# Kernel tuning notes

Hardware: AMD Instinct MI355X
Metric: run time of the kernel (lower is better)

## Reference

```python
import jax, jax.numpy as jnp
import numpy as np

B, L, IN, HID, D3 = 32, 8192, 512, 512, 128

def setup_inputs() -> dict:
    key = jax.random.key(0)
    ks = jax.random.split(key, 7)
    s_in = 1.0 / np.sqrt(IN)
    s_h = 1.0 / np.sqrt(HID)
    return {
        'inputs': jax.random.normal(ks[0], (B, IN), jnp.float32),
        'context': jax.random.normal(ks[1], (B, L, HID), jnp.float32),
        'Wi': jax.random.uniform(ks[2], (D3, IN), jnp.float32, -s_in, s_in),
        'bi': jax.random.uniform(ks[3], (D3,), jnp.float32, -s_in, s_in),
        'Wh': jax.random.uniform(ks[4], (D3, HID), jnp.float32, -s_h, s_h),
        'bh': jax.random.uniform(ks[5], (D3,), jnp.float32, -s_h, s_h),
        'V': jax.random.uniform(ks[6], (D3,), jnp.float32, -1.0, 1.0),
    }

def reference(inputs, context, Wi, bi, Wh, bh, V):
    # inputs: (B, IN) -> (B, 1, D3); context: (B, L, HID) -> (B, L, D3)
    q = (inputs @ Wi.T + bi)[:, None, :]
    k = jnp.einsum('blh,dh->bld', context, Wh) + bh
    a = jnp.tanh(q + k)                              # (B, L, D3)
    att_row = jnp.einsum('bld,d->bl', a, V)[:, None, :]  # (B, 1, L)
    # NOTE: original applies softmax over dim=1 (the singleton dim) -> all ones.
    att = jax.nn.softmax(att_row, axis=1).squeeze(1)     # (B, L), faithful quirk
    return (att_row, att)
```

## Files before the change

kernel.cpp:

```cpp
#include <hip/hip_runtime.h>

typedef __attribute__((ext_vector_type(8))) short short8;
typedef __attribute__((ext_vector_type(8))) unsigned short ushort8;
typedef __attribute__((ext_vector_type(4))) float f32x4;

#define B_   32
#define L_   8192
#define IN_  512
#define HID_ 512
#define D3_  128

static __device__ __forceinline__ short f2bf(float f) {
    return __builtin_bit_cast(short, (__bf16)f);
}
static __device__ __forceinline__ unsigned short f2bfu(float f) {
    return __builtin_bit_cast(unsigned short, (__bf16)f);
}

static __device__ __forceinline__ void gload_lds16(const void* g, void* l) {
    __builtin_amdgcn_global_load_lds(
        (const __attribute__((address_space(1))) unsigned int*)g,
        (__attribute__((address_space(3))) unsigned int*)l, 16, 0, 0);
}

__global__ void prep_whb2(const float* __restrict__ wh, unsigned short* __restrict__ whb2) {
    int u = blockIdx.x * 256 + threadIdx.x;
    int lane = u & 63;
    int nt   = (u >> 6) & 7;
    int ks   = u >> 9;
    int col  = nt * 16 + (lane & 15);
    int k0   = ks * 32 + (lane >> 4) * 8;
    const float* src = wh + col * HID_ + k0;
    float4 a = *(const float4*)(src);
    float4 b = *(const float4*)(src + 4);
    unsigned short* d = whb2 + (size_t)u * 8;
    d[0] = f2bfu(a.x); d[1] = f2bfu(a.y); d[2] = f2bfu(a.z); d[3] = f2bfu(a.w);
    d[4] = f2bfu(b.x); d[5] = f2bfu(b.y); d[6] = f2bfu(b.z); d[7] = f2bfu(b.w);
}

__global__ void prep_qpb(const float* __restrict__ inputs, const float* __restrict__ Wi,
                         const float* __restrict__ bi, const float* __restrict__ bh,
                         float* __restrict__ qpb) {
    int b = blockIdx.x;
    int d = threadIdx.x;
    float acc = bi[d] + bh[d];
    const float* xr = inputs + b * IN_;
    const float* wr = Wi + d * IN_;
    #pragma unroll 4
    for (int i = 0; i < IN_; i += 4) {
        float4 x = *(const float4*)(xr + i);
        float4 w = *(const float4*)(wr + i);
        acc += x.x * w.x + x.y * w.y + x.z * w.z + x.w * w.w;
    }
    qpb[b * D3_ + d] = acc;
}

__global__ __launch_bounds__(512) void attn_main(
    const float* __restrict__ ctx, const unsigned short* __restrict__ whb2,
    const float* __restrict__ qpb, const float* __restrict__ V,
    float* __restrict__ out)
{
    __shared__ unsigned short whs[D3_ * HID_];
    __shared__ float cbuf[2][4096];

    const int tid = threadIdx.x;

    #pragma unroll
    for (int p = 0; p < 16; ++p) {
        int m = p * 512 + tid;
        *(ushort8*)((char*)whs + (size_t)m * 16) = *(const ushort8*)(whb2 + (size_t)m * 8);
    }
    __syncthreads();

    const int lane = tid & 63;
    const int w    = tid >> 6;
    const int cb   = lane & 15;
    const int g    = lane >> 4;

    const char* bptr = (const char*)whs + lane * 16;

    const char* gsrc = (const char*)(ctx
        + ((size_t)blockIdx.x * 1024 + w * 16 + (lane & 15)) * (size_t)HID_)
        + (lane >> 4) * 32;
    char* ldst = (char*)cbuf + w * 2048 + lane * 16;
    const char* aptr = (const char*)cbuf + w * 2048 + lane * 16;

    const int b = blockIdx.x >> 3;

    float vv[8], qv[8];
    #pragma unroll
    for (int nt = 0; nt < 8; ++nt) {
        vv[nt] = V[nt * 16 + cb];
        qv[nt] = qpb[b * D3_ + nt * 16 + cb];
    }

#define STAGE(CC) { \
    const char* g0_ = gsrc + (size_t)((CC) >> 4) * (128 * HID_ * 4) + ((CC) & 15) * 128; \
    char* l0_ = ldst + (((CC) & 1) ? 16384 : 0); \
    gload_lds16(g0_, l0_); \
    gload_lds16(g0_ + 16, l0_ + 1024); }

    STAGE(0)
    STAGE(1)

    #pragma unroll 1
    for (int t = 0; t < 8; ++t) {
        f32x4 acc[8];
        #pragma unroll
        for (int nt = 0; nt < 8; ++nt) acc[nt] = (f32x4){0.f, 0.f, 0.f, 0.f};

        #pragma unroll
        for (int kk = 0; kk < 16; ++kk) {
            const int c = t * 16 + kk;
            if (c < 127) asm volatile("s_waitcnt vmcnt(2)" ::: "memory");
            else         asm volatile("s_waitcnt vmcnt(0)" ::: "memory");

            const char* ap = aptr + ((c & 1) ? 16384 : 0);
            const f32x4 a0 = *(const f32x4*)(ap);
            const f32x4 a1 = *(const f32x4*)(ap + 1024);
            short8 aA;
            aA[0] = f2bf(a0[0]); aA[1] = f2bf(a0[1]); aA[2] = f2bf(a0[2]); aA[3] = f2bf(a0[3]);
            aA[4] = f2bf(a1[0]); aA[5] = f2bf(a1[1]); aA[6] = f2bf(a1[2]); aA[7] = f2bf(a1[3]);

            const char* bp = bptr + kk * 8192;
            #pragma unroll
            for (int nt = 0; nt < 8; ++nt) {
                const short8 bb = *(const short8*)(bp + nt * 1024);
                acc[nt] = __builtin_amdgcn_mfma_f32_16x16x32_bf16(aA, bb, acc[nt], 0, 0, 0);
            }
            asm volatile("s_waitcnt lgkmcnt(0)" ::: "memory");

            if (kk == 15) {
                float s0 = 0.f, s1 = 0.f, s2 = 0.f, s3 = 0.f;
                #pragma unroll
                for (int nt = 0; nt < 8; ++nt) {
                    const float q = qv[nt], vn = vv[nt];
                    s0 += (1.f - 2.f / (__expf(2.f * (acc[nt][0] + q)) + 1.f)) * vn;
                    s1 += (1.f - 2.f / (__expf(2.f * (acc[nt][1] + q)) + 1.f)) * vn;
                    s2 += (1.f - 2.f / (__expf(2.f * (acc[nt][2] + q)) + 1.f)) * vn;
                    s3 += (1.f - 2.f / (__expf(2.f * (acc[nt][3] + q)) + 1.f)) * vn;
                }
                #pragma unroll
                for (int m = 1; m < 16; m <<= 1) {
                    s0 += __shfl_xor(s0, m, 64);
                    s1 += __shfl_xor(s1, m, 64);
                    s2 += __shfl_xor(s2, m, 64);
                    s3 += __shfl_xor(s3, m, 64);
                }
                if (cb == 0) {
                    const size_t row0 = (size_t)blockIdx.x * 1024 + (size_t)t * 128 + w * 16;
                    const size_t off_ = row0 + (size_t)g * 4;
                    *(float4*)(out + off_) = make_float4(s0, s1, s2, s3);
                    *(float4*)(out + (size_t)B_ * L_ + off_) = make_float4(1.f, 1.f, 1.f, 1.f);
                }
            }
            if (c + 2 < 128) STAGE(c + 2)
        }
    }
#undef STAGE
}

extern "C" void kernel_launch(void* const* d_in, const int* in_sizes, int n_in,
                              void* d_out, int out_size, void* d_ws, size_t ws_size,
                              hipStream_t stream) {
    const float* inputs  = (const float*)d_in[0];
    const float* context = (const float*)d_in[1];
    const float* Wi      = (const float*)d_in[2];
    const float* bi      = (const float*)d_in[3];
    const float* Wh      = (const float*)d_in[4];
    const float* bh      = (const float*)d_in[5];
    const float* V       = (const float*)d_in[6];
    float* out = (float*)d_out;

    unsigned short* whb2 = (unsigned short*)d_ws;
    float* qpb = (float*)((char*)d_ws + (size_t)D3_ * HID_ * 2);

    prep_whb2<<<32, 256, 0, stream>>>(Wh, whb2);
    prep_qpb<<<B_, D3_, 0, stream>>>(inputs, Wi, bi, bh, qpb);
    attn_main<<<256, 512, 0, stream>>>(context, whb2, qpb, V, out);
}
```

Before: 132.0 us.

## Load context directly into registers with double-buffered prefetch instead of LDS staging

Replaces the global-to-LDS async staging of context rows with direct float4 global loads into registers, double-buffered two k-steps ahead, including prefetch across tile boundaries. It removes the per-step vmcnt and lgkmcnt waits and the LDS round trip for activations, and uses sched_group_barrier to interleave the LDS weight reads with the MFMAs. The added register pressure and reliance on the compiler's waitcnt insertion could cause stalls if the load latency is not hidden. The loads are also less coalesced, since each lane reads a 32-byte chunk from a different row.

```diff
diff --git a/kernel.cpp b/kernel.cpp
--- a/kernel.cpp
+++ b/kernel.cpp
@@ -15,12 +15,6 @@
 }
 static __device__ __forceinline__ unsigned short f2bfu(float f) {
     return __builtin_bit_cast(unsigned short, (__bf16)f);
-}
-
-static __device__ __forceinline__ void gload_lds16(const void* g, void* l) {
-    __builtin_amdgcn_global_load_lds(
-        (const __attribute__((address_space(1))) unsigned int*)g,
-        (__attribute__((address_space(3))) unsigned int*)l, 16, 0, 0);
 }
 
 __global__ void prep_whb2(const float* __restrict__ wh, unsigned short* __restrict__ whb2) {
@@ -61,7 +55,6 @@
     float* __restrict__ out)
 {
     __shared__ unsigned short whs[D3_ * HID_];
-    __shared__ float cbuf[2][4096];
 
     const int tid = threadIdx.x;
 
@@ -79,11 +72,7 @@
 
     const char* bptr = (const char*)whs + lane * 16;
 
-    const char* gsrc = (const char*)(ctx
-        + ((size_t)blockIdx.x * 1024 + w * 16 + (lane & 15)) * (size_t)HID_)
-        + (lane >> 4) * 32;
-    char* ldst = (char*)cbuf + w * 2048 + lane * 16;
-    const char* aptr = (const char*)cbuf + w * 2048 + lane * 16;
+    const float* pL = ctx + ((size_t)blockIdx.x * 1024 + w * 16 + cb) * (size_t)HID_ + g * 8;
 
     const int b = blockIdx.x >> 3;
 
@@ -94,70 +83,74 @@
         qv[nt] = qpb[b * D3_ + nt * 16 + cb];
     }
 
-#define STAGE(CC) { \
-    const char* g0_ = gsrc + (size_t)((CC) >> 4) * (128 * HID_ * 4) + ((CC) & 15) * 128; \
-    char* l0_ = ldst + (((CC) & 1) ? 16384 : 0); \
-    gload_lds16(g0_, l0_); \
-    gload_lds16(g0_ + 16, l0_ + 1024); }
+#define DOSTEP(PA, PB, KK) { \
+    short8 aA; \
+    aA[0] = f2bf(PA.x); aA[1] = f2bf(PA.y); aA[2] = f2bf(PA.z); aA[3] = f2bf(PA.w); \
+    aA[4] = f2bf(PB.x); aA[5] = f2bf(PB.y); aA[6] = f2bf(PB.z); aA[7] = f2bf(PB.w); \
+    if ((KK) < 14) { \
+        PA = *(const float4*)(pT + ((KK) + 2) * 32); \
+        PB = *(const float4*)(pT + ((KK) + 2) * 32 + 4); \
+    } else { \
+        PA = *(const float4*)(pN + ((KK) - 14) * 32); \
+        PB = *(const float4*)(pN + ((KK) - 14) * 32 + 4); \
+    } \
+    __builtin_amdgcn_sched_barrier(0); \
+    _Pragma("unroll") \
+    for (int nt = 0; nt < 8; ++nt) { \
+        const short8 bb = *(const short8*)(bptr + (KK) * 8192 + nt * 1024); \
+        acc[nt] = __builtin_amdgcn_mfma_f32_16x16x32_bf16(aA, bb, acc[nt], 0, 0, 0); \
+    } \
+    _Pragma("unroll") \
+    for (int q8 = 0; q8 < 8; ++q8) { \
+        __builtin_amdgcn_sched_group_barrier(0x100, 1, 0);  \
+        __builtin_amdgcn_sched_group_barrier(0x008, 1, 0);  \
+    } }
 
-    STAGE(0)
-    STAGE(1)
+    float4 E0 = *(const float4*)(pL);        float4 E1 = *(const float4*)(pL + 4);
+    float4 O0 = *(const float4*)(pL + 32);   float4 O1 = *(const float4*)(pL + 36);
 
     #pragma unroll 1
     for (int t = 0; t < 8; ++t) {
+        const float* pT = pL + (size_t)t * (128 * HID_);
+        const float* pN = (t < 7) ? (pT + 128 * HID_) : pL;
+
         f32x4 acc[8];
         #pragma unroll
         for (int nt = 0; nt < 8; ++nt) acc[nt] = (f32x4){0.f, 0.f, 0.f, 0.f};
 
+        DOSTEP(E0, E1, 0)   DOSTEP(O0, O1, 1)
+        DOSTEP(E0, E1, 2)   DOSTEP(O0, O1, 3)
+        DOSTEP(E0, E1, 4)   DOSTEP(O0, O1, 5)
+        DOSTEP(E0, E1, 6)   DOSTEP(O0, O1, 7)
+        DOSTEP(E0, E1, 8)   DOSTEP(O0, O1, 9)
+        DOSTEP(E0, E1, 10)  DOSTEP(O0, O1, 11)
+        DOSTEP(E0, E1, 12)  DOSTEP(O0, O1, 13)
+        DOSTEP(E0, E1, 14)  DOSTEP(O0, O1, 15)
+
+        float s0 = 0.f, s1 = 0.f, s2 = 0.f, s3 = 0.f;
         #pragma unroll
-        for (int kk = 0; kk < 16; ++kk) {
-            const int c = t * 16 + kk;
-            if (c < 127) asm volatile("s_waitcnt vmcnt(2)" ::: "memory");
-            else         asm volatile("s_waitcnt vmcnt(0)" ::: "memory");
-
-            const char* ap = aptr + ((c & 1) ? 16384 : 0);
-            const f32x4 a0 = *(const f32x4*)(ap);
-            const f32x4 a1 = *(const f32x4*)(ap + 1024);
-            short8 aA;
-            aA[0] = f2bf(a0[0]); aA[1] = f2bf(a0[1]); aA[2] = f2bf(a0[2]); aA[3] = f2bf(a0[3]);
-            aA[4] = f2bf(a1[0]); aA[5] = f2bf(a1[1]); aA[6] = f2bf(a1[2]); aA[7] = f2bf(a1[3]);
-
-            const char* bp = bptr + kk * 8192;
-            #pragma unroll
-            for (int nt = 0; nt < 8; ++nt) {
-                const short8 bb = *(const short8*)(bp + nt * 1024);
-                acc[nt] = __builtin_amdgcn_mfma_f32_16x16x32_bf16(aA, bb, acc[nt], 0, 0, 0);
-            }
-            asm volatile("s_waitcnt lgkmcnt(0)" ::: "memory");
-
-            if (kk == 15) {
-                float s0 = 0.f, s1 = 0.f, s2 = 0.f, s3 = 0.f;
-                #pragma unroll
-                for (int nt = 0; nt < 8; ++nt) {
-                    const float q = qv[nt], vn = vv[nt];
-                    s0 += (1.f - 2.f / (__expf(2.f * (acc[nt][0] + q)) + 1.f)) * vn;
-                    s1 += (1.f - 2.f / (__expf(2.f * (acc[nt][1] + q)) + 1.f)) * vn;
-                    s2 += (1.f - 2.f / (__expf(2.f * (acc[nt][2] + q)) + 1.f)) * vn;
-                    s3 += (1.f - 2.f / (__expf(2.f * (acc[nt][3] + q)) + 1.f)) * vn;
-                }
-                #pragma unroll
-                for (int m = 1; m < 16; m <<= 1) {
-                    s0 += __shfl_xor(s0, m, 64);
-                    s1 += __shfl_xor(s1, m, 64);
-                    s2 += __shfl_xor(s2, m, 64);
-                    s3 += __shfl_xor(s3, m, 64);
-                }
-                if (cb == 0) {
-                    const size_t row0 = (size_t)blockIdx.x * 1024 + (size_t)t * 128 + w * 16;
-                    const size_t off_ = row0 + (size_t)g * 4;
-                    *(float4*)(out + off_) = make_float4(s0, s1, s2, s3);
-                    *(float4*)(out + (size_t)B_ * L_ + off_) = make_float4(1.f, 1.f, 1.f, 1.f);
-                }
-            }
-            if (c + 2 < 128) STAGE(c + 2)
+        for (int nt = 0; nt < 8; ++nt) {
+            const float q = qv[nt], vn = vv[nt];
+            s0 += (1.f - 2.f / (__expf(2.f * (acc[nt][0] + q)) + 1.f)) * vn;
+            s1 += (1.f - 2.f / (__expf(2.f * (acc[nt][1] + q)) + 1.f)) * vn;
+            s2 += (1.f - 2.f / (__expf(2.f * (acc[nt][2] + q)) + 1.f)) * vn;
+            s3 += (1.f - 2.f / (__expf(2.f * (acc[nt][3] + q)) + 1.f)) * vn;
+        }
+        #pragma unroll
+        for (int m = 1; m < 16; m <<= 1) {
+            s0 += __shfl_xor(s0, m, 64);
+            s1 += __shfl_xor(s1, m, 64);
+            s2 += __shfl_xor(s2, m, 64);
+            s3 += __shfl_xor(s3, m, 64);
+        }
+        if (cb == 0) {
+            const size_t row0 = (size_t)blockIdx.x * 1024 + (size_t)t * 128 + w * 16;
+            const size_t off_ = row0 + (size_t)g * 4;
+            *(float4*)(out + off_) = make_float4(s0, s1, s2, s3);
+            *(float4*)(out + (size_t)B_ * L_ + off_) = make_float4(1.f, 1.f, 1.f, 1.f);
         }
     }
-#undef STAGE
+#undef DOSTEP
 }
 
 extern "C" void kernel_launch(void* const* d_in, const int* in_sizes, int n_in,
```

New measurement: 140.6 us. 1.07x slower.
